# Performance work log

Measured on AMD Instinct MI355X. Metric: run time of the kernel, lower is better.

The kernel has to match this reference:

```python
import jax, jax.numpy as jnp
import numpy as np

D_MODEL = 1024
H = 16
D_K = D_MODEL // H
B = 2
S = 2048


def setup_inputs() -> dict:
    key = jax.random.key(0)
    ks = jax.random.split(key, 12)
    s = 1.0 / np.sqrt(D_MODEL)
    inp = {
        "q": jax.random.normal(ks[0], (B, S, D_MODEL), jnp.float32),
        "k": jax.random.normal(ks[1], (B, S, D_MODEL), jnp.float32),
        "v": jax.random.normal(ks[2], (B, S, D_MODEL), jnp.float32),
        "mask": jnp.ones((B, 1, S, S), jnp.int32),
        "w_q": jax.random.normal(ks[3], (D_MODEL, D_MODEL), jnp.float32) * s,
        "b_q": jax.random.normal(ks[4], (D_MODEL,), jnp.float32) * 0.02,
        "w_k": jax.random.normal(ks[5], (D_MODEL, D_MODEL), jnp.float32) * s,
        "b_k": jax.random.normal(ks[6], (D_MODEL,), jnp.float32) * 0.02,
        "w_v": jax.random.normal(ks[7], (D_MODEL, D_MODEL), jnp.float32) * s,
        "b_v": jax.random.normal(ks[8], (D_MODEL,), jnp.float32) * 0.02,
        "w_o": jax.random.normal(ks[9], (D_MODEL, D_MODEL), jnp.float32) * s,
        "b_o": jax.random.normal(ks[10], (D_MODEL,), jnp.float32) * 0.02,
    }
    return inp


def reference(q, k, v, mask, w_q, b_q, w_k, b_k, w_v, b_v, w_o, b_o):
    # Linear projections (torch Linear: x @ W^T + b)
    query = q @ w_q.T + b_q
    key = k @ w_k.T + b_k
    value = v @ w_v.T + b_v
    # (B,S,D) -> (B,H,S,d_k)
    def split_heads(x):
        return x.reshape(B, S, H, D_K).transpose(0, 2, 1, 3)
    query, key, value = split_heads(query), split_heads(key), split_heads(value)
    scale = 1.0 / jnp.sqrt(jnp.asarray(D_K, q.dtype))
    scores = jnp.einsum('bhqd,bhkd->bhqk', query, key) * scale
    scores = jnp.where(mask == 0, jnp.asarray(-jnp.inf, scores.dtype), scores)
    attn = jax.nn.softmax(scores, axis=-1)  # dropout is identity in eval
    x = jnp.einsum('bhqk,bhkd->bhqd', attn, value)
    x = x.transpose(0, 2, 1, 3).reshape(B, S, D_MODEL)
    return x @ w_o.T + b_o
```

## Files before the change

### kernel.cpp

```cpp
#include <hip/hip_runtime.h>

#define DM 1024
#define NH 16
#define DK 64
#define BB 2
#define SS 2048
#define MM (BB*SS)

typedef unsigned short u16;
typedef __bf16 bf16x8 __attribute__((ext_vector_type(8)));
typedef __bf16 bf16x4 __attribute__((ext_vector_type(4)));
typedef unsigned short u16x8 __attribute__((ext_vector_type(8)));
typedef unsigned short u16x4 __attribute__((ext_vector_type(4)));
typedef float f32x4 __attribute__((ext_vector_type(4)));
typedef unsigned int u32;
typedef unsigned int u32x2 __attribute__((ext_vector_type(2)));

__device__ __forceinline__ u16 f2bf(float f) {
  union { float f; unsigned u; } v; v.f = f;
  unsigned r = v.u + 0x7FFFu + ((v.u >> 16) & 1u);
  return (u16)(r >> 16);
}

__device__ __forceinline__ bf16x8 ld8(const u16* p) {
  return __builtin_bit_cast(bf16x8, *(const u16x8*)p);
}

__device__ __forceinline__ void async16(const void* g, void* l) {
  __builtin_amdgcn_global_load_lds(
      (const __attribute__((address_space(1))) void*)g,
      (__attribute__((address_space(3))) void*)l, 16, 0, 0);
}

struct CvtArgs {
  const float* src[7];
  u16* dst[7];
  int n[7];
};

__global__ __launch_bounds__(256) void cvt_kernel(CvtArgs a) {
  const int which = blockIdx.y;
  const long i = (long)(blockIdx.x * 256 + threadIdx.x) * 8;
  if (i >= a.n[which]) return;
  const float* s = a.src[which] + i;
  float4 x = *(const float4*)s;
  float4 y = *(const float4*)(s + 4);
  u16x8 o;
  o[0]=f2bf(x.x); o[1]=f2bf(x.y); o[2]=f2bf(x.z); o[3]=f2bf(x.w);
  o[4]=f2bf(y.x); o[5]=f2bf(y.y); o[6]=f2bf(y.z); o[7]=f2bf(y.w);
  *(u16x8*)(a.dst[which] + i) = o;
}

struct QKVArgs {
  const u16* A[3];
  const u16* W[3];
  const float* bias[3];
  u16* out[3];
};

__global__ __launch_bounds__(256, 4) void qkv_gemm(QKVArgs ga) {
  __shared__ __align__(16) u16 As[2][128 * 32];
  __shared__ __align__(16) u16 Bs[2][128 * 32];
  const int z = blockIdx.z;
  const u16* __restrict__ A = ga.A[z];
  const u16* __restrict__ W = ga.W[z];
  const float* __restrict__ bias = ga.bias[z];
  const float outScale = (z == 0) ? 0.125f * 1.44269504f : 1.0f;

  const int tid = threadIdx.x;
  const int lane = tid & 63;
  const int wave = tid >> 6;
  const int m16 = lane & 15, q4 = lane >> 4;
  const int wr = wave >> 1, wc = wave & 1;
  const long row0 = (long)blockIdx.y * 128;
  const long col0 = (long)blockIdx.x * 128;

  f32x4 acc[4][4] = {};
  const int r0 = tid >> 2;
  const int r1 = r0 + 64;
  const int cc = (((tid & 3) ^ ((tid >> 3) & 3))) * 8;

  const u16* Ar0 = A + (row0 + r0) * DM + cc;
  const u16* Ar1 = A + (row0 + r1) * DM + cc;
  const u16* Wr0 = W + (col0 + r0) * DM + cc;
  const u16* Wr1 = W + (col0 + r1) * DM + cc;

  async16(Ar0, &As[0][tid * 8]);
  async16(Ar1, &As[0][(tid + 256) * 8]);
  async16(Wr0, &Bs[0][tid * 8]);
  async16(Wr1, &Bs[0][(tid + 256) * 8]);

  for (int k0 = 0; k0 < DM; k0 += 32) {
    const int cur = (k0 >> 5) & 1;
    __syncthreads();
    if (k0 + 32 < DM) {
      async16(Ar0 + k0 + 32, &As[1 - cur][tid * 8]);
      async16(Ar1 + k0 + 32, &As[1 - cur][(tid + 256) * 8]);
      async16(Wr0 + k0 + 32, &Bs[1 - cur][tid * 8]);
      async16(Wr1 + k0 + 32, &Bs[1 - cur][(tid + 256) * 8]);
    }
    bf16x8 af[4], bfr[4];
#pragma unroll
    for (int i = 0; i < 4; ++i) {
      const int row = wr*64 + i*16 + m16;
      af[i] = ld8(&As[cur][row * 32 + (q4 ^ ((row >> 1) & 3)) * 8]);
    }
#pragma unroll
    for (int j = 0; j < 4; ++j) {
      const int row = wc*64 + j*16 + m16;
      bfr[j] = ld8(&Bs[cur][row * 32 + (q4 ^ ((row >> 1) & 3)) * 8]);
    }
#pragma unroll
    for (int i = 0; i < 4; ++i)
#pragma unroll
      for (int j = 0; j < 4; ++j)
        acc[i][j] = __builtin_amdgcn_mfma_f32_16x16x32_bf16(af[i], bfr[j], acc[i][j], 0, 0, 0);
  }

  if (z != 2) {
    u16* out = ga.out[z];
#pragma unroll
    for (int j = 0; j < 4; ++j) {
      const long col = col0 + wc*64 + j*16 + m16;
      const float bv = bias[col];
#pragma unroll
      for (int i = 0; i < 4; ++i)
#pragma unroll
        for (int r = 0; r < 4; ++r) {
          const long row = row0 + wr*64 + i*16 + q4*4 + r;
          out[row * DM + col] = f2bf((acc[i][j][r] + bv) * outScale);
        }
    }
  } else {
    u16* VT = ga.out[2];
#pragma unroll
    for (int j = 0; j < 4; ++j) {
      const long col = col0 + wc*64 + j*16 + m16;
      const long h = col >> 6, d = col & 63;
      const float bv = bias[col];
#pragma unroll
      for (int i = 0; i < 4; ++i) {
        const long row = row0 + wr*64 + i*16 + q4*4;
        const long b = row >> 11, s = row & 2047;
        u16x4 pk;
#pragma unroll
        for (int r = 0; r < 4; ++r) pk[r] = f2bf(acc[i][j][r] + bv);
        *(u16x4*)&VT[((b*16 + h)*64 + d) * 2048 + s] = pk;
      }
    }
  }
}

__global__ __launch_bounds__(256, 2) void gemm_o(
    const u16* __restrict__ A, const u16* __restrict__ W,
    const float* __restrict__ bias, float* __restrict__ Cout) {
  __shared__ __align__(16) u16 As[3][64 * 64];
  __shared__ __align__(16) u16 Bs[3][128 * 64];
  const int tid = threadIdx.x;
  const int lane = tid & 63;
  const int wave = tid >> 6;
  const int m16 = lane & 15, q4 = lane >> 4;
  const int wr = wave >> 1, wc = wave & 1;
  const long row0 = (long)blockIdx.y * 64;
  const long col0 = (long)blockIdx.x * 128;

  f32x4 acc[2][4] = {};

  const int ra0 = tid >> 3, pa0 = tid & 7;
  const int ra1 = (tid + 256) >> 3;
  const u16* Asrc0 = A + (row0 + ra0) * DM + (pa0 ^ (ra0 & 7)) * 8;
  const u16* Asrc1 = A + (row0 + ra1) * DM + (pa0 ^ (ra1 & 7)) * 8;
  const u16* Wsrc[4];
#pragma unroll
  for (int t = 0; t < 4; ++t) {
    const int c = tid + t * 256;
    const int row = c >> 3, p = c & 7;
    Wsrc[t] = W + (col0 + row) * DM + (p ^ (row & 7)) * 8;
  }

  auto stage = [&](int kk, int b) {
    async16(Asrc0 + kk * 64, &As[b][tid * 8]);
    async16(Asrc1 + kk * 64, &As[b][(tid + 256) * 8]);
#pragma unroll
    for (int t = 0; t < 4; ++t)
      async16(Wsrc[t] + kk * 64, &Bs[b][(tid + t * 256) * 8]);
  };
  auto compute = [&](int b) {
#pragma unroll
    for (int kc = 0; kc < 2; ++kc) {
      bf16x8 af[2], bf[4];
#pragma unroll
      for (int i = 0; i < 2; ++i) {
        const int ra = wr*32 + i*16 + m16;
        af[i] = ld8(&As[b][ra*64 + ((kc*4 + q4) ^ (ra & 7)) * 8]);
      }
#pragma unroll
      for (int j = 0; j < 4; ++j) {
        const int rb = wc*64 + j*16 + m16;
        bf[j] = ld8(&Bs[b][rb*64 + ((kc*4 + q4) ^ (rb & 7)) * 8]);
      }
#pragma unroll
      for (int i = 0; i < 2; ++i)
#pragma unroll
        for (int j = 0; j < 4; ++j)
          acc[i][j] = __builtin_amdgcn_mfma_f32_16x16x32_bf16(bf[j], af[i], acc[i][j], 0, 0, 0);
    }
  };

  stage(0, 0);
  stage(1, 1);

  for (int kt = 0; kt < 14; ++kt) {
    asm volatile("s_waitcnt vmcnt(6)" ::: "memory");
    __builtin_amdgcn_s_barrier();
    stage(kt + 2, (kt + 2) % 3);
    compute(kt % 3);
  }
  asm volatile("s_waitcnt vmcnt(6)" ::: "memory");
  __builtin_amdgcn_s_barrier();
  compute(2);
  asm volatile("s_waitcnt vmcnt(0)" ::: "memory");
  __builtin_amdgcn_s_barrier();
  compute(0);

#pragma unroll
  for (int i = 0; i < 2; ++i) {
    const long row = row0 + wr*32 + i*16 + m16;
#pragma unroll
    for (int j = 0; j < 4; ++j) {
      const long colb = col0 + wc*64 + j*16 + q4*4;
      const float4 bv = *(const float4*)&bias[colb];
      float4 o;
      o.x = acc[i][j][0] + bv.x;
      o.y = acc[i][j][1] + bv.y;
      o.z = acc[i][j][2] + bv.z;
      o.w = acc[i][j][3] + bv.w;
      *(float4*)&Cout[row * DM + colb] = o;
    }
  }
}

__global__ __launch_bounds__(512, 4) void attn_kernel(
    const u16* __restrict__ Qp, const u16* __restrict__ Kp,
    const u16* __restrict__ Vt, u16* __restrict__ Xa) {
  __shared__ __align__(16) u16 Ks[2][128 * 64];
  __shared__ __align__(16) u16 Vs[2][64 * 128];
  __shared__ float Ls[4][2][2][16];

  const int tid = threadIdx.x;
  const int lane = tid & 63;
  const int wave = tid >> 6;
  const int m16 = lane & 15, q4 = lane >> 4;
  const int qw = wave & 3;
  const int jh = wave >> 2;
  const int bh = blockIdx.y;
  const int b = bh >> 4, h = bh & 15;
  const int qbase = blockIdx.x * 128 + qw * 32;
  const size_t base = (size_t)b * SS * DM + (size_t)h * DK;
  const size_t baseV = (size_t)bh * 64 * 2048;

  const int kr = tid >> 3;
  const int kb = kr & 31;
  const int ksrc = (kr & ~31) + ((kb >> 2) & 3) * 8 + ((kb >> 4) << 2) + (kb & 3);
  const int kswz = ((tid & 7) ^ (kr & 7)) * 8;
  const u16* KpS0 = Kp + base + (size_t)ksrc * DM + kswz;
  const u16* KpS1 = KpS0 + (size_t)64 * DM;
  const int vr = tid >> 4;
  const int vswz = ((tid & 15) ^ (vr & 15)) * 8;
  const u16* VtS0 = Vt + baseV + (size_t)vr * 2048 + vswz;
  const u16* VtS1 = VtS0 + (size_t)32 * 2048;

  bf16x8 qf[2][2];
#pragma unroll
  for (int qg = 0; qg < 2; ++qg) {
    const u16* qptr = Qp + base + (size_t)(qbase + qg*16 + m16) * DM;
    qf[qg][0] = ld8(qptr + q4 * 8);
    qf[qg][1] = ld8(qptr + 32 + q4 * 8);
  }
  bf16x8 vb1;
  {
    u16x8 w;
    const u16 o = (m16 == 0) ? (u16)0x3F80 : (u16)0;
#pragma unroll
    for (int i = 0; i < 8; ++i) w[i] = o;
    vb1 = __builtin_bit_cast(bf16x8, w);
  }

  f32x4 accO[2][4] = {};
  f32x4 accL[2] = {};

  async16(KpS0, &Ks[0][tid * 8]);
  async16(KpS1, &Ks[0][(tid + 512) * 8]);
  async16(VtS0, &Vs[0][tid * 8]);
  async16(VtS1, &Vs[0][(tid + 512) * 8]);

  for (int kt = 0; kt < SS / 128; ++kt) {
    const int cur = kt & 1;
    __syncthreads();
    if (kt + 1 < SS / 128) {
      const size_t off = (size_t)(kt + 1) * 128;
      u16* kd = &Ks[1 - cur][0];
      u16* vd = &Vs[1 - cur][0];
      async16(KpS0 + off * DM, kd + tid * 8);
      async16(KpS1 + off * DM, kd + (tid + 512) * 8);
      async16(VtS0 + off, vd + tid * 8);
      async16(VtS1 + off, vd + (tid + 512) * 8);
    }
    const u16* Kc = &Ks[cur][0];
    const u16* Vc = &Vs[cur][0];

    f32x4 st[2][4] = {};
    __builtin_amdgcn_s_setprio(1);
#pragma unroll
    for (int t = 0; t < 4; ++t) {
      const int rr = (jh*4 + t) * 16 + m16;
      bf16x8 kf0 = ld8(&Kc[rr * 64 + ((q4    ) ^ (m16 & 7)) * 8]);
      bf16x8 kf1 = ld8(&Kc[rr * 64 + ((4 + q4) ^ (m16 & 7)) * 8]);
#pragma unroll
      for (int qg = 0; qg < 2; ++qg) {
        st[qg][t] = __builtin_amdgcn_mfma_f32_16x16x32_bf16(kf0, qf[qg][0], st[qg][t], 0, 0, 0);
        st[qg][t] = __builtin_amdgcn_mfma_f32_16x16x32_bf16(kf1, qf[qg][1], st[qg][t], 0, 0, 0);
      }
    }
    __builtin_amdgcn_s_setprio(0);

    bf16x8 af32[2][2];
#pragma unroll
    for (int qg = 0; qg < 2; ++qg)
#pragma unroll
      for (int tt = 0; tt < 2; ++tt) {
        const f32x4 s0 = st[qg][tt*2], s1 = st[qg][tt*2 + 1];
        bf16x8 v;
        v[0] = (__bf16)__builtin_amdgcn_exp2f(s0[0]);
        v[1] = (__bf16)__builtin_amdgcn_exp2f(s0[1]);
        v[2] = (__bf16)__builtin_amdgcn_exp2f(s0[2]);
        v[3] = (__bf16)__builtin_amdgcn_exp2f(s0[3]);
        v[4] = (__bf16)__builtin_amdgcn_exp2f(s1[0]);
        v[5] = (__bf16)__builtin_amdgcn_exp2f(s1[1]);
        v[6] = (__bf16)__builtin_amdgcn_exp2f(s1[2]);
        v[7] = (__bf16)__builtin_amdgcn_exp2f(s1[3]);
        af32[qg][tt] = v;
      }

    __builtin_amdgcn_s_setprio(1);
#pragma unroll
    for (int dt = 0; dt < 4; ++dt) {
      const int dr = dt * 16 + m16;
#pragma unroll
      for (int tt = 0; tt < 2; ++tt) {
        const int lc = jh*8 + tt*4 + q4;
        bf16x8 vb = ld8(&Vc[dr * 128 + (lc ^ (dr & 15)) * 8]);
#pragma unroll
        for (int qg = 0; qg < 2; ++qg)
          accO[qg][dt] = __builtin_amdgcn_mfma_f32_16x16x32_bf16(af32[qg][tt], vb, accO[qg][dt], 0, 0, 0);
      }
    }
#pragma unroll
    for (int tt = 0; tt < 2; ++tt)
#pragma unroll
      for (int qg = 0; qg < 2; ++qg)
        accL[qg] = __builtin_amdgcn_mfma_f32_16x16x32_bf16(af32[qg][tt], vb1, accL[qg], 0, 0, 0);
    __builtin_amdgcn_s_setprio(0);
  }

  __syncthreads();
  float* P0 = (float*)&Ks[0][0];
  float* P1 = (float*)&Vs[0][0];
  if (m16 == 0) {
#pragma unroll
    for (int qg = 0; qg < 2; ++qg)
#pragma unroll
      for (int r = 0; r < 4; ++r)
        Ls[qw][qg][jh][q4 * 4 + r] = accL[qg][r];
  }
  if (jh) {
#pragma unroll
    for (int dt = 0; dt < 4; ++dt) {
      *(f32x4*)&P0[(qw*4 + dt) * 256 + lane * 4] = accO[0][dt];
      *(f32x4*)&P1[(qw*4 + dt) * 256 + lane * 4] = accO[1][dt];
    }
  }
  __syncthreads();
  if (!jh) {
#pragma unroll
    for (int dt = 0; dt < 4; ++dt) {
      accO[0][dt] += *(const f32x4*)&P0[(qw*4 + dt) * 256 + lane * 4];
      accO[1][dt] += *(const f32x4*)&P1[(qw*4 + dt) * 256 + lane * 4];
    }

#pragma unroll
    for (int qg = 0; qg < 2; ++qg)
#pragma unroll
      for (int r = 0; r < 4; ++r) {
        const float lr = Ls[qw][qg][0][q4*4 + r] + Ls[qw][qg][1][q4*4 + r];
        const float inv = 1.0f / lr;
        const size_t row = (size_t)b * SS + qbase + qg*16 + q4 * 4 + r;
#pragma unroll
        for (int dt = 0; dt < 4; ++dt)
          Xa[row * DM + h * DK + dt * 16 + m16] = f2bf(accO[qg][dt][r] * inv);
      }
  }
}

extern "C" void kernel_launch(void* const* d_in, const int* in_sizes, int n_in,
                              void* d_out, int out_size, void* d_ws, size_t ws_size,
                              hipStream_t stream) {
  const float* q   = (const float*)d_in[0];
  const float* k   = (const float*)d_in[1];
  const float* v   = (const float*)d_in[2];
  const float* w_q = (const float*)d_in[4];
  const float* b_q = (const float*)d_in[5];
  const float* w_k = (const float*)d_in[6];
  const float* b_k = (const float*)d_in[7];
  const float* w_v = (const float*)d_in[8];
  const float* b_v = (const float*)d_in[9];
  const float* w_o = (const float*)d_in[10];
  const float* b_o = (const float*)d_in[11];

  u16* Wq = (u16*)d_ws;
  u16* Wk = Wq + (1 << 20);
  u16* Wv = Wk + (1 << 20);
  u16* Wo = Wv + (1 << 20);
  u16* Qb = Wo + (1 << 20);
  u16* Kb = Qb + (4 << 20);
  u16* Vb = Kb + (4 << 20);
  u16* Qp = Vb + (4 << 20);
  u16* Kp = Qp + (4 << 20);
  u16* VTg = Kp + (4 << 20);
  u16* Xa = Qb;

  CvtArgs ca;
  ca.src[0] = q;   ca.dst[0] = Qb; ca.n[0] = MM * DM;
  ca.src[1] = k;   ca.dst[1] = Kb; ca.n[1] = MM * DM;
  ca.src[2] = v;   ca.dst[2] = Vb; ca.n[2] = MM * DM;
  ca.src[3] = w_q; ca.dst[3] = Wq; ca.n[3] = DM * DM;
  ca.src[4] = w_k; ca.dst[4] = Wk; ca.n[4] = DM * DM;
  ca.src[5] = w_v; ca.dst[5] = Wv; ca.n[5] = DM * DM;
  ca.src[6] = w_o; ca.dst[6] = Wo; ca.n[6] = DM * DM;
  cvt_kernel<<<dim3(2048, 7), 256, 0, stream>>>(ca);

  QKVArgs ga;
  ga.A[0] = Qb; ga.A[1] = Kb; ga.A[2] = Vb;
  ga.W[0] = Wq; ga.W[1] = Wk; ga.W[2] = Wv;
  ga.bias[0] = b_q; ga.bias[1] = b_k; ga.bias[2] = b_v;
  ga.out[0] = Qp; ga.out[1] = Kp; ga.out[2] = VTg;
  qkv_gemm<<<dim3(8, 32, 3), 256, 0, stream>>>(ga);

  attn_kernel<<<dim3(16, 32), 512, 0, stream>>>(Qp, Kp, VTg, Xa);

  gemm_o<<<dim3(8, 64), 256, 0, stream>>>(Xa, Wo, b_o, (float*)d_out);
}
```

Measured before the change: 232.8 us.

## Fuse fp32-to-bf16 activation conversion into QKV GEMM A-tile loading

Removes the separate conversion pass over the q/k/v activations. The QKV GEMM now loads fp32 A tiles into registers, converts them to bf16, and writes them to swizzled LDS, with the loads software-pipelined one k-step ahead of the MFMA compute. The cvt kernel now only converts the four weight matrices, and uses the native __bf16 cast instead of the manual rounding helper. This saves writing and re-reading 3x8MB of bf16 intermediates, in exchange for double the global A traffic inside the GEMM, higher register pressure, and synchronous loads in place of async global-to-LDS copies.

Result: slower. 242.6 us (+4.2%).

```diff
diff --git a/kernel.cpp b/kernel.cpp
--- a/kernel.cpp
+++ b/kernel.cpp
@@ -32,27 +32,29 @@
       (__attribute__((address_space(3))) void*)l, 16, 0, 0);
 }
 
+__device__ __forceinline__ u16x8 cvt8(float4 x, float4 y) {
+  bf16x8 v;
+  v[0] = (__bf16)x.x; v[1] = (__bf16)x.y; v[2] = (__bf16)x.z; v[3] = (__bf16)x.w;
+  v[4] = (__bf16)y.x; v[5] = (__bf16)y.y; v[6] = (__bf16)y.z; v[7] = (__bf16)y.w;
+  return __builtin_bit_cast(u16x8, v);
+}
+
 struct CvtArgs {
-  const float* src[7];
-  u16* dst[7];
-  int n[7];
+  const float* src[4];
+  u16* dst[4];
 };
 
 __global__ __launch_bounds__(256) void cvt_kernel(CvtArgs a) {
   const int which = blockIdx.y;
   const long i = (long)(blockIdx.x * 256 + threadIdx.x) * 8;
-  if (i >= a.n[which]) return;
   const float* s = a.src[which] + i;
   float4 x = *(const float4*)s;
   float4 y = *(const float4*)(s + 4);
-  u16x8 o;
-  o[0]=f2bf(x.x); o[1]=f2bf(x.y); o[2]=f2bf(x.z); o[3]=f2bf(x.w);
-  o[4]=f2bf(y.x); o[5]=f2bf(y.y); o[6]=f2bf(y.z); o[7]=f2bf(y.w);
-  *(u16x8*)(a.dst[which] + i) = o;
+  *(u16x8*)(a.dst[which] + i) = cvt8(x, y);
 }
 
 struct QKVArgs {
-  const u16* A[3];
+  const float* A[3];
   const u16* W[3];
   const float* bias[3];
   u16* out[3];
@@ -62,7 +64,7 @@
   __shared__ __align__(16) u16 As[2][128 * 32];
   __shared__ __align__(16) u16 Bs[2][128 * 32];
   const int z = blockIdx.z;
-  const u16* __restrict__ A = ga.A[z];
+  const float* __restrict__ A = ga.A[z];
   const u16* __restrict__ W = ga.W[z];
   const float* __restrict__ bias = ga.bias[z];
   const float outScale = (z == 0) ? 0.125f * 1.44269504f : 1.0f;
@@ -78,43 +80,62 @@
   f32x4 acc[4][4] = {};
   const int r0 = tid >> 2;
   const int r1 = r0 + 64;
-  const int cc = (((tid & 3) ^ ((tid >> 3) & 3))) * 8;
-
-  const u16* Ar0 = A + (row0 + r0) * DM + cc;
-  const u16* Ar1 = A + (row0 + r1) * DM + cc;
+  const int c4 = tid & 3;
+  const int sw = (r0 >> 1) & 3;
+  const int slot = (c4 ^ sw) * 8;
+  const int cc = (c4 ^ sw) * 8;
+
+  const float* Af0 = A + (row0 + r0) * DM + c4 * 8;
+  const float* Af1 = A + (row0 + r1) * DM + c4 * 8;
   const u16* Wr0 = W + (col0 + r0) * DM + cc;
   const u16* Wr1 = W + (col0 + r1) * DM + cc;
 
-  async16(Ar0, &As[0][tid * 8]);
-  async16(Ar1, &As[0][(tid + 256) * 8]);
+  float4 a0, a1, a2, a3;
+  auto loadA = [&](int kk) {
+    const float* p0 = Af0 + kk * 32;
+    a0 = *(const float4*)p0; a1 = *(const float4*)(p0 + 4);
+    const float* p1 = Af1 + kk * 32;
+    a2 = *(const float4*)p1; a3 = *(const float4*)(p1 + 4);
+  };
+  auto writeA = [&](int b) {
+    *(u16x8*)&As[b][r0 * 32 + slot] = cvt8(a0, a1);
+    *(u16x8*)&As[b][r1 * 32 + slot] = cvt8(a2, a3);
+  };
+  auto compute = [&](int b) {
+    bf16x8 af[4], bfr[4];
+#pragma unroll
+    for (int i = 0; i < 4; ++i) {
+      const int row = wr*64 + i*16 + m16;
+      af[i] = ld8(&As[b][row * 32 + (q4 ^ ((row >> 1) & 3)) * 8]);
+    }
+#pragma unroll
+    for (int j = 0; j < 4; ++j) {
+      const int row = wc*64 + j*16 + m16;
+      bfr[j] = ld8(&Bs[b][row * 32 + (q4 ^ ((row >> 1) & 3)) * 8]);
+    }
+#pragma unroll
+    for (int i = 0; i < 4; ++i)
+#pragma unroll
+      for (int j = 0; j < 4; ++j)
+        acc[i][j] = __builtin_amdgcn_mfma_f32_16x16x32_bf16(af[i], bfr[j], acc[i][j], 0, 0, 0);
+  };
+
+  loadA(0);
   async16(Wr0, &Bs[0][tid * 8]);
   async16(Wr1, &Bs[0][(tid + 256) * 8]);
-
-  for (int k0 = 0; k0 < DM; k0 += 32) {
-    const int cur = (k0 >> 5) & 1;
+  writeA(0);
+  __syncthreads();
+
+  for (int kt = 0; kt < 32; ++kt) {
+    const int cur = kt & 1;
+    if (kt + 1 < 32) {
+      loadA(kt + 1);
+      async16(Wr0 + (kt + 1) * 32, &Bs[1 - cur][tid * 8]);
+      async16(Wr1 + (kt + 1) * 32, &Bs[1 - cur][(tid + 256) * 8]);
+    }
+    compute(cur);
+    if (kt + 1 < 32) writeA(1 - cur);
     __syncthreads();
-    if (k0 + 32 < DM) {
-      async16(Ar0 + k0 + 32, &As[1 - cur][tid * 8]);
-      async16(Ar1 + k0 + 32, &As[1 - cur][(tid + 256) * 8]);
-      async16(Wr0 + k0 + 32, &Bs[1 - cur][tid * 8]);
-      async16(Wr1 + k0 + 32, &Bs[1 - cur][(tid + 256) * 8]);
-    }
-    bf16x8 af[4], bfr[4];
-#pragma unroll
-    for (int i = 0; i < 4; ++i) {
-      const int row = wr*64 + i*16 + m16;
-      af[i] = ld8(&As[cur][row * 32 + (q4 ^ ((row >> 1) & 3)) * 8]);
-    }
-#pragma unroll
-    for (int j = 0; j < 4; ++j) {
-      const int row = wc*64 + j*16 + m16;
-      bfr[j] = ld8(&Bs[cur][row * 32 + (q4 ^ ((row >> 1) & 3)) * 8]);
-    }
-#pragma unroll
-    for (int i = 0; i < 4; ++i)
-#pragma unroll
-      for (int j = 0; j < 4; ++j)
-        acc[i][j] = __builtin_amdgcn_mfma_f32_16x16x32_bf16(af[i], bfr[j], acc[i][j], 0, 0, 0);
   }
 
   if (z != 2) {
@@ -421,26 +442,20 @@
   u16* Wk = Wq + (1 << 20);
   u16* Wv = Wk + (1 << 20);
   u16* Wo = Wv + (1 << 20);
-  u16* Qb = Wo + (1 << 20);
-  u16* Kb = Qb + (4 << 20);
-  u16* Vb = Kb + (4 << 20);
-  u16* Qp = Vb + (4 << 20);
+  u16* Qp = Wo + (1 << 20);
   u16* Kp = Qp + (4 << 20);
   u16* VTg = Kp + (4 << 20);
-  u16* Xa = Qb;
+  u16* Xa = VTg + (4 << 20);
 
   CvtArgs ca;
-  ca.src[0] = q;   ca.dst[0] = Qb; ca.n[0] = MM * DM;
-  ca.src[1] = k;   ca.dst[1] = Kb; ca.n[1] = MM * DM;
-  ca.src[2] = v;   ca.dst[2] = Vb; ca.n[2] = MM * DM;
-  ca.src[3] = w_q; ca.dst[3] = Wq; ca.n[3] = DM * DM;
-  ca.src[4] = w_k; ca.dst[4] = Wk; ca.n[4] = DM * DM;
-  ca.src[5] = w_v; ca.dst[5] = Wv; ca.n[5] = DM * DM;
-  ca.src[6] = w_o; ca.dst[6] = Wo; ca.n[6] = DM * DM;
-  cvt_kernel<<<dim3(2048, 7), 256, 0, stream>>>(ca);
+  ca.src[0] = w_q; ca.dst[0] = Wq;
+  ca.src[1] = w_k; ca.dst[1] = Wk;
+  ca.src[2] = w_v; ca.dst[2] = Wv;
+  ca.src[3] = w_o; ca.dst[3] = Wo;
+  cvt_kernel<<<dim3(512, 4), 256, 0, stream>>>(ca);
 
   QKVArgs ga;
-  ga.A[0] = Qb; ga.A[1] = Kb; ga.A[2] = Vb;
+  ga.A[0] = q; ga.A[1] = k; ga.A[2] = v;
   ga.W[0] = Wq; ga.W[1] = Wk; ga.W[2] = Wv;
   ga.bias[0] = b_q; ga.bias[1] = b_k; ga.bias[2] = b_v;
   ga.out[0] = Qp; ga.out[1] = Kp; ga.out[2] = VTg;
```
